# Performance work log

Measured on AMD Instinct MI355X. Metric: run time of the kernel, lower is better.

The kernel has to match this reference:

```python
import jax, jax.numpy as jnp
import numpy as np
from jax import lax

EPS = 1e-6


def layernorm2d(x, w, b):
    # channel LayerNorm over dim C of NCHW (biased variance), matching LayerNormFunction
    mu = jnp.mean(x, axis=1, keepdims=True)
    var = jnp.mean((x - mu) ** 2, axis=1, keepdims=True)
    y = (x - mu) * lax.rsqrt(var + EPS)
    return w[None, :, None, None] * y + b[None, :, None, None]


def conv1x1(x, W, b):
    # x: (N,C,H,W), W: (O,C), b: (O,)
    return jnp.einsum('nchw,oc->nohw', x, W) + b[None, :, None, None]


def conv3x3(x, W, b):
    # W: (O,I,3,3)
    y = lax.conv_general_dilated(x, W, window_strides=(1, 1), padding='SAME',
                                 dimension_numbers=('NCHW', 'OIHW', 'NCHW'))
    return y + b[None, :, None, None]


def avg_pool3x3(x):
    # torch F.avg_pool2d k=3, s=1, p=1, count_include_pad=True -> always divide by 9
    s = lax.reduce_window(x, 0.0, lax.add, (1, 1, 3, 3), (1, 1, 1, 1),
                          [(0, 0), (0, 0), (1, 1), (1, 1)])
    return s / 9.0


def setup_inputs() -> dict:
    key = jax.random.key(0)
    N, C, H, W = 8, 64, 128, 256
    ks = jax.random.split(key, 12)
    d = {
        'x_l': jax.random.normal(ks[0], (N, C, H, W), jnp.float32),
        'x_r': jax.random.normal(ks[1], (N, C, H, W), jnp.float32),
        'nl_w': jnp.ones((C,), jnp.float32),
        'nl_b': jnp.zeros((C,), jnp.float32),
        'nr_w': jnp.ones((C,), jnp.float32),
        'nr_b': jnp.zeros((C,), jnp.float32),
        'Wq_l': jax.random.normal(ks[2], (C, C), jnp.float32) * 0.05,
        'bq_l': jax.random.normal(ks[3], (C,), jnp.float32) * 0.05,
        'Wq_r': jax.random.normal(ks[4], (C, C), jnp.float32) * 0.05,
        'bq_r': jax.random.normal(ks[5], (C,), jnp.float32) * 0.05,
        'Wv_r': jax.random.normal(ks[6], (C, C), jnp.float32) * 0.05,
        'bv_r': jax.random.normal(ks[7], (C,), jnp.float32) * 0.05,
        'beta': jax.random.normal(ks[8], (1, C, 1, 1), jnp.float32) * 0.1,
        'gamma': jax.random.normal(ks[9], (1, C, 1, 1), jnp.float32) * 0.1,
        'W_hf': jax.random.normal(ks[10], (C, C, 3, 3), jnp.float32) * 0.02,
        'b_hf': jax.random.normal(ks[11], (C,), jnp.float32) * 0.02,
    }
    return d


def reference(x_l, x_r, nl_w, nl_b, nr_w, nr_b, Wq_l, bq_l, Wq_r, bq_r,
              Wv_r, bv_r, beta, gamma, W_hf, b_hf):
    C = x_l.shape[1]
    scale = C ** (-0.5)

    # Projections (1x1 convs); Q_l, Q_r, V_r as (N,H,W,C)
    Q_l = jnp.transpose(conv1x1(layernorm2d(x_l, nl_w, nl_b), Wq_l, bq_l), (0, 2, 3, 1))
    Q_r = jnp.transpose(conv1x1(layernorm2d(x_r, nr_w, nr_b), Wq_r, bq_r), (0, 2, 3, 1))
    V_r = jnp.transpose(conv1x1(x_r, Wv_r, bv_r), (0, 2, 3, 1))

    # Per-scanline cross attention: (N,H,W,W)
    attn = jnp.einsum('nhwc,nhvc->nhwv', Q_l, Q_r) * scale
    attn = jax.nn.softmax(attn, axis=-1)
    F_r2l = jnp.einsum('nhwv,nhvc->nhwc', attn, V_r)  # (N,H,W,C)
    F_r2l = jnp.transpose(F_r2l, (0, 3, 1, 2)) * beta  # (N,C,H,W)

    # High-frequency branch
    hf = conv3x3(x_r - avg_pool3x3(x_r), W_hf, b_hf)

    return x_l + F_r2l + gamma * hf
```

## Files before the change

### kernel.cpp

```cpp
#include <hip/hip_runtime.h>
#include <hip/hip_bf16.h>

#define N_ 8
#define C_ 64
#define H_ 128
#define W_ 256
#define HW_ (H_*W_)
#define CHW_ (C_*H_*W_)

typedef unsigned int u32;
typedef unsigned short u16;
typedef float f32x4 __attribute__((ext_vector_type(4)));
typedef short bf16x8 __attribute__((ext_vector_type(8)));

__device__ __forceinline__ float blo(u32 u) { return __uint_as_float(u << 16); }
__device__ __forceinline__ float bhi(u32 u) { return __uint_as_float(u & 0xffff0000u); }
__device__ __forceinline__ u16 f2bf(float f) {
    u32 u = __float_as_uint(f);
    u32 lsb = (u >> 16) & 1u;
    u += 0x7fffu + lsb;
    return (u16)(u >> 16);
}
__device__ __forceinline__ u32 pack2(float a, float b) {
    return (u32)f2bf(a) | ((u32)f2bf(b) << 16);
}
__device__ __forceinline__ int rmap(int px) {
    return (px & 0xF8) | ((px + (px >> 3)) & 7);
}

__global__ __launch_bounds__(512, 2) void k_fused(
    const float* __restrict__ xl, const float* __restrict__ xr,
    const float* __restrict__ nlw, const float* __restrict__ nlb,
    const float* __restrict__ nrw, const float* __restrict__ nrb,
    const float* __restrict__ Wql, const float* __restrict__ bql,
    const float* __restrict__ Wqr, const float* __restrict__ bqr,
    const float* __restrict__ Wvr, const float* __restrict__ bvr,
    const float* __restrict__ beta, float* __restrict__ out)
{
    __shared__ u32 B1[8192];
    __shared__ u32 B2[8192];
    __shared__ float muA[256], rsA[256];
    __shared__ float SlA[64], BlA[64], SrA[64], BrA[64], BvA[64];
    const int tid  = threadIdx.x;
    const int lane = tid & 63, wv = tid >> 6;
    const int l15  = lane & 15, kg = lane >> 4;
    const int mw   = wv & 3;
    const int nh   = wv >> 2;
    const int blk  = blockIdx.x;
    const int n = blk >> 7, h = blk & 127;
    const size_t gbase = (size_t)n*CHW_ + (size_t)h*W_;

    if (tid < 64) {
        const int o = tid;
        float sl = 0.f, bl = bql[o], sr = 0.f, br = bqr[o];
        for (int c = 0; c < 64; ++c) {
            float wl = Wql[o*64+c], wr = Wqr[o*64+c];
            sl += wl * nlw[c];
            bl += wl * nlb[c];
            sr += wr * nrw[c];
            br += wr * nrb[c];
        }
        SlA[o] = sl; BlA[o] = bl; SrA[o] = sr; BrA[o] = br; BvA[o] = bvr[o];
    }

    const int oA = mw*16 + l15;
    bf16x8 aL[2], aR[2], aV[2];
    #pragma unroll
    for (int hf = 0; hf < 2; ++hf) {
        bf16x8 tl, tr, tv;
        #pragma unroll
        for (int j = 0; j < 8; ++j) {
            const int c = hf*32 + kg*8 + j;
            tl[j] = (short)f2bf(Wql[oA*64+c] * nlw[c]);
            tr[j] = (short)f2bf(Wqr[oA*64+c] * nrw[c]);
            tv[j] = (short)f2bf(Wvr[oA*64+c]);
        }
        aL[hf] = tl; aR[hf] = tr; aV[hf] = tv;
    }

    const int schunk = tid >> 6;
    const int sj     = tid & 63;

    {
        const int c0 = schunk*8;
        float4 v[8];
        #pragma unroll
        for (int e = 0; e < 8; ++e)
            v[e] = *(const float4*)(xl + gbase + (size_t)(c0+e)*HW_ + sj*4);
        #pragma unroll
        for (int t = 0; t < 4; ++t) {
            const int px = sj*4 + t;
            const int r = rmap(px);
            u32 q0,q1,q2,q3;
            const float* f0 = (const float*)&v[0]; const float* f1 = (const float*)&v[1];
            const float* f2 = (const float*)&v[2]; const float* f3 = (const float*)&v[3];
            const float* f4 = (const float*)&v[4]; const float* f5 = (const float*)&v[5];
            const float* f6 = (const float*)&v[6]; const float* f7 = (const float*)&v[7];
            asm("v_cvt_pk_bf16_f32 %0, %1, %2" : "=v"(q0) : "v"(f0[t]), "v"(f1[t]));
            asm("v_cvt_pk_bf16_f32 %0, %1, %2" : "=v"(q1) : "v"(f2[t]), "v"(f3[t]));
            asm("v_cvt_pk_bf16_f32 %0, %1, %2" : "=v"(q2) : "v"(f4[t]), "v"(f5[t]));
            asm("v_cvt_pk_bf16_f32 %0, %1, %2" : "=v"(q3) : "v"(f6[t]), "v"(f7[t]));
            uint4 pv; pv.x=q0; pv.y=q1; pv.z=q2; pv.w=q3;
            *(uint4*)&B1[r*32 + ((schunk ^ (r&7))<<2)] = pv;
        }
    }
    float4 vr2[8];
    {
        const int c0 = schunk*8;
        #pragma unroll
        for (int e = 0; e < 8; ++e)
            vr2[e] = *(const float4*)(xr + gbase + (size_t)(c0+e)*HW_ + sj*4);
    }
    __syncthreads();
    if (tid < 256) {
        const int px = tid;
        const int r = rmap(px);
        float sum = 0.f, ssq = 0.f;
        #pragma unroll
        for (int c8 = 0; c8 < 8; ++c8) {
            uint4 val = *(const uint4*)&B1[r*32 + ((c8 ^ (r&7))<<2)];
            const u32* wp = (const u32*)&val;
            #pragma unroll
            for (int q = 0; q < 4; ++q) {
                float a = blo(wp[q]), b = bhi(wp[q]);
                sum += a + b; ssq += a*a + b*b;
            }
        }
        float mu = sum * (1.f/64.f);
        float var = ssq * (1.f/64.f) - mu*mu;
        muA[px] = mu;
        rsA[px] = rsqrtf(var + 1e-6f);
    }
    __syncthreads();
    {
        float Sv[4], Bv[4];
        #pragma unroll
        for (int r4 = 0; r4 < 4; ++r4) {
            Sv[r4] = SlA[mw*16 + kg*4 + r4];
            Bv[r4] = BlA[mw*16 + kg*4 + r4];
        }
        #pragma unroll
        for (int nt2 = 0; nt2 < 8; ++nt2) {
            const int nt = nh*8 + nt2;
            const int px = nt*16 + l15;
            const int r = rmap(px);
            f32x4 d = {0.f,0.f,0.f,0.f};
            #pragma unroll
            for (int hf = 0; hf < 2; ++hf) {
                bf16x8 b = *(const bf16x8*)&B1[r*32 + (((hf*4+kg) ^ (r&7))<<2)];
                d = __builtin_amdgcn_mfma_f32_16x16x32_bf16(aL[hf], b, d, 0, 0, 0);
            }
            const float mu = muA[px], rs = rsA[px];
            uint2 pv;
            pv.x = pack2(rs*(d[0] - mu*Sv[0]) + Bv[0], rs*(d[1] - mu*Sv[1]) + Bv[1]);
            pv.y = pack2(rs*(d[2] - mu*Sv[2]) + Bv[2], rs*(d[3] - mu*Sv[3]) + Bv[3]);
            const int ci = (mw*2 + (kg>>1)) ^ (px & 7);
            *(uint2*)&B2[px*32 + (ci<<2) + (kg&1)*2] = pv;
        }
    }
    __syncthreads();

    bf16x8 qf[2][2];
    #pragma unroll
    for (int ntq = 0; ntq < 2; ++ntq)
        #pragma unroll
        for (int ci = 0; ci < 2; ++ci) {
            const int q = wv*32 + ntq*16 + l15;
            qf[ntq][ci] = *(const bf16x8*)&B2[q*32 + (((ci*4+kg) ^ (q&7))<<2)];
        }
    {
        #pragma unroll
        for (int t = 0; t < 4; ++t) {
            const int px = sj*4 + t;
            const int r = rmap(px);
            u32 q0,q1,q2,q3;
            const float* f0 = (const float*)&vr2[0]; const float* f1 = (const float*)&vr2[1];
            const float* f2 = (const float*)&vr2[2]; const float* f3 = (const float*)&vr2[3];
            const float* f4 = (const float*)&vr2[4]; const float* f5 = (const float*)&vr2[5];
            const float* f6 = (const float*)&vr2[6]; const float* f7 = (const float*)&vr2[7];
            asm("v_cvt_pk_bf16_f32 %0, %1, %2" : "=v"(q0) : "v"(f0[t]), "v"(f1[t]));
            asm("v_cvt_pk_bf16_f32 %0, %1, %2" : "=v"(q1) : "v"(f2[t]), "v"(f3[t]));
            asm("v_cvt_pk_bf16_f32 %0, %1, %2" : "=v"(q2) : "v"(f4[t]), "v"(f5[t]));
            asm("v_cvt_pk_bf16_f32 %0, %1, %2" : "=v"(q3) : "v"(f6[t]), "v"(f7[t]));
            uint4 pv; pv.x=q0; pv.y=q1; pv.z=q2; pv.w=q3;
            *(uint4*)&B1[r*32 + ((schunk ^ (r&7))<<2)] = pv;
        }
    }
    __syncthreads();
    if (tid < 256) {
        const int px = tid;
        const int r = rmap(px);
        float sum = 0.f, ssq = 0.f;
        #pragma unroll
        for (int c8 = 0; c8 < 8; ++c8) {
            uint4 val = *(const uint4*)&B1[r*32 + ((c8 ^ (r&7))<<2)];
            const u32* wp = (const u32*)&val;
            #pragma unroll
            for (int q = 0; q < 4; ++q) {
                float a = blo(wp[q]), b = bhi(wp[q]);
                sum += a + b; ssq += a*a + b*b;
            }
        }
        float mu = sum * (1.f/64.f);
        float var = ssq * (1.f/64.f) - mu*mu;
        muA[px] = mu;
        rsA[px] = rsqrtf(var + 1e-6f);
    }
    __syncthreads();

    u32 hq[8][2], hv[8][2];
    {
        float Sv[4], Bv[4];
        #pragma unroll
        for (int r4 = 0; r4 < 4; ++r4) {
            Sv[r4] = SrA[mw*16 + kg*4 + r4];
            Bv[r4] = BrA[mw*16 + kg*4 + r4];
        }
        const int chv = mw*16 + l15;
        const float vbias = BvA[chv];
        #pragma unroll
        for (int nt2 = 0; nt2 < 8; ++nt2) {
            const int nt = nh*8 + nt2;
            const int px = nt*16 + l15;
            const int r = rmap(px);
            bf16x8 bX[2];
            #pragma unroll
            for (int hf = 0; hf < 2; ++hf)
                bX[hf] = *(const bf16x8*)&B1[r*32 + (((hf*4+kg) ^ (r&7))<<2)];
            f32x4 dq = {0.f,0.f,0.f,0.f};
            f32x4 dv = {0.f,0.f,0.f,0.f};
            #pragma unroll
            for (int hf = 0; hf < 2; ++hf) {
                dq = __builtin_amdgcn_mfma_f32_16x16x32_bf16(aR[hf], bX[hf], dq, 0, 0, 0);
                dv = __builtin_amdgcn_mfma_f32_16x16x32_bf16(bX[hf], aV[hf], dv, 0, 0, 0);
            }
            const float mu = muA[px], rs = rsA[px];
            hq[nt2][0] = pack2(rs*(dq[0] - mu*Sv[0]) + Bv[0], rs*(dq[1] - mu*Sv[1]) + Bv[1]);
            hq[nt2][1] = pack2(rs*(dq[2] - mu*Sv[2]) + Bv[2], rs*(dq[3] - mu*Sv[3]) + Bv[3]);
            hv[nt2][0] = pack2(dv[0] + vbias, dv[1] + vbias);
            hv[nt2][1] = pack2(dv[2] + vbias, dv[3] + vbias);
        }
    }
    __syncthreads();
    {
        const int chv = mw*16 + l15;
        u16* Vts16 = (u16*)B2;
        #pragma unroll
        for (int nt2 = 0; nt2 < 8; ++nt2) {
            const int nt = nh*8 + nt2;
            const int px = nt*16 + l15;
            const int ciq = (mw*2 + (kg>>1)) ^ (px & 7);
            uint2 pq; pq.x = hq[nt2][0]; pq.y = hq[nt2][1];
            *(uint2*)&B1[px*32 + (ciq<<2) + (kg&1)*2] = pq;
            uint2 pw; pw.x = hv[nt2][0]; pw.y = hv[nt2][1];
            const int swz = (nt*2 + (kg>>1)) ^ (chv & 7);
            *(uint2*)&Vts16[chv*256 + (swz<<3) + (kg&1)*4] = pw;
        }
    }
    __syncthreads();

    f32x4 oacc[2][4];
    #pragma unroll
    for (int a = 0; a < 2; ++a)
        #pragma unroll
        for (int b = 0; b < 4; ++b)
            oacc[a][b] = (f32x4){0.f,0.f,0.f,0.f};
    float lsum[2] = {0.f,0.f};
    const uint4* KsR = (const uint4*)B1;
    const u16* Vts = (const u16*)B2;
    const int srcA = ((2*kg) & 3)*16 + l15;

    for (int kb = 0; kb < 8; ++kb) {
        f32x4 st[2][2];
        #pragma unroll
        for (int mt = 0; mt < 2; ++mt)
            #pragma unroll
            for (int nt = 0; nt < 2; ++nt)
                st[mt][nt] = (f32x4){0.f,0.f,0.f,0.f};
        #pragma unroll
        for (int ci = 0; ci < 2; ++ci) {
            bf16x8 a0 = *(const bf16x8*)&KsR[(kb*32 +      l15)*8 + ((ci*4 + kg) ^ (l15 & 7))];
            bf16x8 a1 = *(const bf16x8*)&KsR[(kb*32 + 16 + l15)*8 + ((ci*4 + kg) ^ (l15 & 7))];
            #pragma unroll
            for (int nt = 0; nt < 2; ++nt) {
                st[0][nt] = __builtin_amdgcn_mfma_f32_16x16x32_bf16(a0, qf[nt][ci], st[0][nt], 0, 0, 0);
                st[1][nt] = __builtin_amdgcn_mfma_f32_16x16x32_bf16(a1, qf[nt][ci], st[1][nt], 0, 0, 0);
            }
        }
        bf16x8 paR[2];
        #pragma unroll
        for (int nt = 0; nt < 2; ++nt) {
            float p00 = __expf(st[0][nt][0]*0.125f);
            float p01 = __expf(st[0][nt][1]*0.125f);
            float p02 = __expf(st[0][nt][2]*0.125f);
            float p03 = __expf(st[0][nt][3]*0.125f);
            float p10 = __expf(st[1][nt][0]*0.125f);
            float p11 = __expf(st[1][nt][1]*0.125f);
            float p12 = __expf(st[1][nt][2]*0.125f);
            float p13 = __expf(st[1][nt][3]*0.125f);
            lsum[nt] += ((p00+p01)+(p02+p03)) + ((p10+p11)+(p12+p13));
            u32 pk00, pk01, pk10, pk11;
            asm("v_cvt_pk_bf16_f32 %0, %1, %2" : "=v"(pk00) : "v"(p00), "v"(p01));
            asm("v_cvt_pk_bf16_f32 %0, %1, %2" : "=v"(pk01) : "v"(p02), "v"(p03));
            asm("v_cvt_pk_bf16_f32 %0, %1, %2" : "=v"(pk10) : "v"(p10), "v"(p11));
            asm("v_cvt_pk_bf16_f32 %0, %1, %2" : "=v"(pk11) : "v"(p12), "v"(p13));
            int a00 = __shfl((int)pk00, srcA, 64);
            int a01 = __shfl((int)pk01, srcA, 64);
            int a10 = __shfl((int)pk10, srcA, 64);
            int a11 = __shfl((int)pk11, srcA, 64);
            int b00 = __shfl((int)pk00, srcA + 16, 64);
            int b01 = __shfl((int)pk01, srcA + 16, 64);
            int b10 = __shfl((int)pk10, srcA + 16, 64);
            int b11 = __shfl((int)pk11, srcA + 16, 64);
            const bool lo = (kg < 2);
            union { u32 u[4]; bf16x8 v; } pu;
            pu.u[0] = (u32)(lo ? a00 : a10);
            pu.u[1] = (u32)(lo ? a01 : a11);
            pu.u[2] = (u32)(lo ? b00 : b10);
            pu.u[3] = (u32)(lo ? b01 : b11);
            paR[nt] = pu.v;
        }
        bf16x8 vb[4];
        #pragma unroll
        for (int nc = 0; nc < 4; ++nc)
            vb[nc] = *(const bf16x8*)&Vts[(nc*16 + l15)*256 + ((kb*4 + kg) ^ (l15 & 7))*8];
        #pragma unroll
        for (int qt = 0; qt < 2; ++qt)
            #pragma unroll
            for (int nc = 0; nc < 4; ++nc)
                oacc[qt][nc] = __builtin_amdgcn_mfma_f32_16x16x32_bf16(paR[qt], vb[nc], oacc[qt][nc], 0, 0, 0);
    }

    #pragma unroll
    for (int nt = 0; nt < 2; ++nt) {
        float s = lsum[nt];
        s += __shfl_xor(s, 16, 64);
        s += __shfl_xor(s, 32, 64);
        lsum[nt] = s;
    }
    float linv[2][4];
    #pragma unroll
    for (int qt = 0; qt < 2; ++qt)
        #pragma unroll
        for (int r = 0; r < 4; ++r)
            linv[qt][r] = 1.0f / __shfl(lsum[qt], kg*4 + r, 64);

    const size_t qbase = gbase + wv*32;
    #pragma unroll
    for (int nc = 0; nc < 4; ++nc) {
        const int ch = nc*16 + l15;
        const float bch = beta[ch];
        #pragma unroll
        for (int qt = 0; qt < 2; ++qt) {
            const size_t gidx = qbase + (size_t)ch*HW_ + qt*16 + kg*4;
            f32x4 vals;
            #pragma unroll
            for (int r = 0; r < 4; ++r)
                vals[r] = bch*(oacc[qt][nc][r]*linv[qt][r]);
            *(f32x4*)&out[gidx] = vals;
        }
    }
}

__global__ __launch_bounds__(256) void k_hipass(
    const float* __restrict__ xr, u16* __restrict__ Tt)
{
    __shared__ u16 Ts[64*256];
    const int bid = blockIdx.x;
    const int blk = (bid & 7)*128 + (bid >> 3);
    const int n = blk >> 7, h = blk & 127;
    const int tid = threadIdx.x;
    const int lane = tid & 63, wv = tid >> 6;
    const float* rowp = xr + (size_t)n*CHW_ + (size_t)h*W_ + lane*4;

    #pragma unroll
    for (int ci = 0; ci < 16; ++ci) {
        const int c = wv*16 + ci;
        const float* pc = rowp + (size_t)c*HW_;
        float ctr0=0.f, ctr1=0.f, ctr2=0.f, ctr3=0.f;
        float s0=0.f, s1=0.f, s2=0.f, s3=0.f;
        #pragma unroll
        for (int dy = -1; dy <= 1; ++dy) {
            const int hh = h + dy;
            float4 v = {0.f,0.f,0.f,0.f};
            if (hh >= 0 && hh < 128) v = *(const float4*)(pc + dy*W_);
            float lft = __shfl_up(v.w, 1);
            float rgt = __shfl_down(v.x, 1);
            if (lane == 0)  lft = 0.f;
            if (lane == 63) rgt = 0.f;
            s0 += lft + v.x + v.y;
            s1 += v.x + v.y + v.z;
            s2 += v.y + v.z + v.w;
            s3 += v.z + v.w + rgt;
            if (dy == 0) { ctr0=v.x; ctr1=v.y; ctr2=v.z; ctr3=v.w; }
        }
        uint2 pv;
        pv.x = pack2(ctr0 - s0*(1.f/9.f), ctr1 - s1*(1.f/9.f));
        pv.y = pack2(ctr2 - s2*(1.f/9.f), ctr3 - s3*(1.f/9.f));
        const int swz = (c >> 3) << 3;
        *(uint2*)&Ts[c*256 + ((lane*4) ^ swz)] = pv;
    }
    __syncthreads();
    uint4* gout = (uint4*)(Tt + (size_t)blk*256*64);
    #pragma unroll
    for (int iter = 0; iter < 8; ++iter) {
        const int lin = iter*256 + tid;
        const int px = lin >> 3, chunk = lin & 7;
        const int pxs = px ^ (chunk << 3);
        u32 w4[4];
        #pragma unroll
        for (int tp = 0; tp < 4; ++tp) {
            const int c0 = chunk*8 + tp*2;
            u16 a = Ts[(c0    )*256 + pxs];
            u16 b = Ts[(c0 + 1)*256 + pxs];
            w4[tp] = (u32)a | ((u32)b << 16);
        }
        uint4 v; v.x=w4[0]; v.y=w4[1]; v.z=w4[2]; v.w=w4[3];
        gout[lin] = v;
    }
}

__device__ __forceinline__ void conv_tile(
    const uint4* __restrict__ buf, const bf16x8* A,
    const float* gv, const float* bv,
    int n, int h, int w0, int mt, int l15, int kg,
    const float* __restrict__ xl, float* __restrict__ out)
{
    f32x4 acc[4] = {{0,0,0,0},{0,0,0,0},{0,0,0,0},{0,0,0,0}};
    #pragma unroll
    for (int s = 0; s < 18; ++s) {
        const int q  = s >> 1;
        const int dy = q / 3, dx = q % 3;
        const int c0 = (s & 1)*4 + kg;
        #pragma unroll
        for (int nt = 0; nt < 4; ++nt) {
            const int wt = nt*16 + l15 + dx;
            bf16x8 b = *(const bf16x8*)&buf[(dy*66 + wt)*8 + (c0 ^ (wt & 7))];
            acc[nt] = __builtin_amdgcn_mfma_f32_16x16x32_bf16(A[s], b, acc[nt], 0, 0, 0);
        }
    }
    #pragma unroll
    for (int nt = 0; nt < 4; ++nt) {
        const int px = w0 + nt*16 + l15;
        #pragma unroll
        for (int r = 0; r < 4; ++r) {
            const int oo = mt*16 + kg*4 + r;
            size_t idx = (size_t)(n*64 + oo)*HW_ + (size_t)h*W_ + px;
            out[idx] = out[idx] + xl[idx] + gv[r]*(acc[nt][r] + bv[r]);
        }
    }
}

__global__ __launch_bounds__(256) void k_conv(
    const u16* __restrict__ Tt, const float* __restrict__ Whf,
    const float* __restrict__ bhf, const float* __restrict__ gam,
    const float* __restrict__ xl, float* __restrict__ out)
{
    __shared__ uint4 Xs[2][1584];
    const int tid  = threadIdx.x;
    const int lane = tid & 63;
    const int mt   = tid >> 6;
    const int l15  = lane & 15;
    const int kg   = lane >> 4;
    const int bid  = blockIdx.x;
    const int blk2 = (bid & 7)*256 + (bid >> 3);
    const int row  = blk2 >> 1, half = blk2 & 1;
    const int n = row >> 7, h = row & 127;
    const int w00 = half*128;
    const int w01 = w00 + 64;

    const int oa = mt*16 + l15;
    bf16x8 A[18];
    #pragma unroll
    for (int s = 0; s < 18; ++s) {
        const int q  = s >> 1;
        const int ib = (s & 1)*32 + kg*8;
        bf16x8 a;
        #pragma unroll
        for (int j = 0; j < 8; ++j) {
            float wv = Whf[(size_t)(oa*64 + ib + j)*9 + q];
            a[j] = (short)f2bf(wv);
        }
        A[s] = a;
    }
    float gv[4], bv[4];
    #pragma unroll
    for (int r = 0; r < 4; ++r) {
        int oo = mt*16 + kg*4 + r;
        gv[r] = gam[oo];
        bv[r] = bhf[oo];
    }

    for (int it = tid; it < 1584; it += 256) {
        int dy    = it / 528;
        int rem   = it - dy*528;
        int wt    = rem >> 3;
        int chunk = rem & 7;
        int hh = h + dy - 1;
        int wg = w00 + wt - 1;
        uint4 v = {0,0,0,0};
        if (hh >= 0 && hh < 128 && wg >= 0 && wg < 256)
            v = *(const uint4*)(Tt + (((size_t)(n*128 + hh)*256 + wg)*64 + chunk*8));
        Xs[0][(dy*66 + wt)*8 + (chunk ^ (wt & 7))] = v;
    }
    __syncthreads();

    uint4 rr[7];
    #pragma unroll
    for (int k = 0; k < 7; ++k) {
        const int it = k*256 + tid;
        if (it < 1584) {
            int dy    = it / 528;
            int rem   = it - dy*528;
            int wt    = rem >> 3;
            int chunk = rem & 7;
            int hh = h + dy - 1;
            int wg = w01 + wt - 1;
            uint4 v = {0,0,0,0};
            if (hh >= 0 && hh < 128 && wg >= 0 && wg < 256)
                v = *(const uint4*)(Tt + (((size_t)(n*128 + hh)*256 + wg)*64 + chunk*8));
            rr[k] = v;
        }
    }

    conv_tile(&Xs[0][0], A, gv, bv, n, h, w00, mt, l15, kg, xl, out);

    #pragma unroll
    for (int k = 0; k < 7; ++k) {
        const int it = k*256 + tid;
        if (it < 1584) {
            int dy    = it / 528;
            int rem   = it - dy*528;
            int wt    = rem >> 3;
            int chunk = rem & 7;
            Xs[1][(dy*66 + wt)*8 + (chunk ^ (wt & 7))] = rr[k];
        }
    }
    __syncthreads();
    conv_tile(&Xs[1][0], A, gv, bv, n, h, w01, mt, l15, kg, xl, out);
}

extern "C" void kernel_launch(void* const* d_in, const int* in_sizes, int n_in,
                              void* d_out, int out_size, void* d_ws, size_t ws_size,
                              hipStream_t stream)
{
    const float* xl   = (const float*)d_in[0];
    const float* xr   = (const float*)d_in[1];
    const float* nlw  = (const float*)d_in[2];
    const float* nlb  = (const float*)d_in[3];
    const float* nrw  = (const float*)d_in[4];
    const float* nrb  = (const float*)d_in[5];
    const float* Wql  = (const float*)d_in[6];
    const float* bql  = (const float*)d_in[7];
    const float* Wqr  = (const float*)d_in[8];
    const float* bqr  = (const float*)d_in[9];
    const float* Wvr  = (const float*)d_in[10];
    const float* bvr  = (const float*)d_in[11];
    const float* beta = (const float*)d_in[12];
    const float* gam  = (const float*)d_in[13];
    const float* Whf  = (const float*)d_in[14];
    const float* bhf  = (const float*)d_in[15];
    float* out = (float*)d_out;

    u16* Tt = (u16*)d_ws;

    k_hipass<<<1024, 256, 0, stream>>>(xr, Tt);
    k_fused<<<1024, 512, 0, stream>>>(xl, xr, nlw, nlb, nrw, nrb,
                                      Wql, bql, Wqr, bqr, Wvr, bvr,
                                      beta, out);
    k_conv<<<2048, 256, 0, stream>>>(Tt, Whf, bhf, gam, xl, out);
}
```

Measured before the change: 193.8 us.

## Merge high-pass kernel into attention kernel via block roles; move x_l residual add

The separate high-pass kernel is folded into the attention kernel as a second block role: odd blocks compute the x_r minus avg-pool bf16 tile, even blocks run attention, so the two workloads share one launch and can overlap on the GPU. The x_l residual add moves from the conv kernel's read-modify-write into the attention epilogue, so the conv kernel no longer reads x_l. This removes one launch and lets the memory-bound high-pass blocks run alongside the compute-heavy attention blocks. In exchange, the high-pass blocks now launch with 512 threads and the large shared-memory footprint of the attention kernel, which may reduce occupancy for that role.

```diff
diff --git a/kernel.cpp b/kernel.cpp
--- a/kernel.cpp
+++ b/kernel.cpp
@@ -28,25 +28,84 @@
     return (px & 0xF8) | ((px + (px >> 3)) & 7);
 }
 
-__global__ __launch_bounds__(512, 2) void k_fused(
+__global__ __launch_bounds__(512, 2) void k_main(
     const float* __restrict__ xl, const float* __restrict__ xr,
     const float* __restrict__ nlw, const float* __restrict__ nlb,
     const float* __restrict__ nrw, const float* __restrict__ nrb,
     const float* __restrict__ Wql, const float* __restrict__ bql,
     const float* __restrict__ Wqr, const float* __restrict__ bqr,
     const float* __restrict__ Wvr, const float* __restrict__ bvr,
-    const float* __restrict__ beta, float* __restrict__ out)
+    const float* __restrict__ beta, u16* __restrict__ Tt,
+    float* __restrict__ out)
 {
     __shared__ u32 B1[8192];
     __shared__ u32 B2[8192];
     __shared__ float muA[256], rsA[256];
     __shared__ float SlA[64], BlA[64], SrA[64], BrA[64], BvA[64];
-    const int tid  = threadIdx.x;
+    const int tid = threadIdx.x;
+    const int bid = blockIdx.x;
+    const int role = bid & 1;
+    const int sub  = bid >> 1;
+
+    if (role == 1) {
+        u16* Ts = (u16*)B1;
+        const int blkh = (sub & 7)*128 + (sub >> 3);
+        const int nh_ = blkh >> 7, hh_ = blkh & 127;
+        const int lane = tid & 63, wvv = tid >> 6;
+        const float* rowp = xr + (size_t)nh_*CHW_ + (size_t)hh_*W_ + lane*4;
+        #pragma unroll
+        for (int ci = 0; ci < 8; ++ci) {
+            const int c = wvv*8 + ci;
+            const float* pc = rowp + (size_t)c*HW_;
+            float ctr0=0.f, ctr1=0.f, ctr2=0.f, ctr3=0.f;
+            float s0=0.f, s1=0.f, s2=0.f, s3=0.f;
+            #pragma unroll
+            for (int dy = -1; dy <= 1; ++dy) {
+                const int hh2 = hh_ + dy;
+                float4 v = {0.f,0.f,0.f,0.f};
+                if (hh2 >= 0 && hh2 < 128) v = *(const float4*)(pc + dy*W_);
+                float lft = __shfl_up(v.w, 1);
+                float rgt = __shfl_down(v.x, 1);
+                if (lane == 0)  lft = 0.f;
+                if (lane == 63) rgt = 0.f;
+                s0 += lft + v.x + v.y;
+                s1 += v.x + v.y + v.z;
+                s2 += v.y + v.z + v.w;
+                s3 += v.z + v.w + rgt;
+                if (dy == 0) { ctr0=v.x; ctr1=v.y; ctr2=v.z; ctr3=v.w; }
+            }
+            uint2 pv;
+            pv.x = pack2(ctr0 - s0*(1.f/9.f), ctr1 - s1*(1.f/9.f));
+            pv.y = pack2(ctr2 - s2*(1.f/9.f), ctr3 - s3*(1.f/9.f));
+            const int swz = (c >> 3) << 3;
+            *(uint2*)&Ts[c*256 + ((lane*4) ^ swz)] = pv;
+        }
+        __syncthreads();
+        uint4* gout = (uint4*)(Tt + (size_t)blkh*256*64);
+        #pragma unroll
+        for (int iter = 0; iter < 4; ++iter) {
+            const int lin = iter*512 + tid;
+            const int px = lin >> 3, chunk = lin & 7;
+            const int pxs = px ^ (chunk << 3);
+            u32 w4[4];
+            #pragma unroll
+            for (int tp = 0; tp < 4; ++tp) {
+                const int c0 = chunk*8 + tp*2;
+                u16 a = Ts[(c0    )*256 + pxs];
+                u16 b = Ts[(c0 + 1)*256 + pxs];
+                w4[tp] = (u32)a | ((u32)b << 16);
+            }
+            uint4 v; v.x=w4[0]; v.y=w4[1]; v.z=w4[2]; v.w=w4[3];
+            gout[lin] = v;
+        }
+        return;
+    }
+
     const int lane = tid & 63, wv = tid >> 6;
     const int l15  = lane & 15, kg = lane >> 4;
     const int mw   = wv & 3;
     const int nh   = wv >> 2;
-    const int blk  = blockIdx.x;
+    const int blk  = sub;
     const int n = blk >> 7, h = blk & 127;
     const size_t gbase = (size_t)n*CHW_ + (size_t)h*W_;
 
@@ -353,70 +412,13 @@
         #pragma unroll
         for (int qt = 0; qt < 2; ++qt) {
             const size_t gidx = qbase + (size_t)ch*HW_ + qt*16 + kg*4;
+            f32x4 x4 = *(const f32x4*)&xl[gidx];
             f32x4 vals;
             #pragma unroll
             for (int r = 0; r < 4; ++r)
-                vals[r] = bch*(oacc[qt][nc][r]*linv[qt][r]);
+                vals[r] = x4[r] + bch*(oacc[qt][nc][r]*linv[qt][r]);
             *(f32x4*)&out[gidx] = vals;
         }
-    }
-}
-
-__global__ __launch_bounds__(256) void k_hipass(
-    const float* __restrict__ xr, u16* __restrict__ Tt)
-{
-    __shared__ u16 Ts[64*256];
-    const int bid = blockIdx.x;
-    const int blk = (bid & 7)*128 + (bid >> 3);
-    const int n = blk >> 7, h = blk & 127;
-    const int tid = threadIdx.x;
-    const int lane = tid & 63, wv = tid >> 6;
-    const float* rowp = xr + (size_t)n*CHW_ + (size_t)h*W_ + lane*4;
-
-    #pragma unroll
-    for (int ci = 0; ci < 16; ++ci) {
-        const int c = wv*16 + ci;
-        const float* pc = rowp + (size_t)c*HW_;
-        float ctr0=0.f, ctr1=0.f, ctr2=0.f, ctr3=0.f;
-        float s0=0.f, s1=0.f, s2=0.f, s3=0.f;
-        #pragma unroll
-        for (int dy = -1; dy <= 1; ++dy) {
-            const int hh = h + dy;
-            float4 v = {0.f,0.f,0.f,0.f};
-            if (hh >= 0 && hh < 128) v = *(const float4*)(pc + dy*W_);
-            float lft = __shfl_up(v.w, 1);
-            float rgt = __shfl_down(v.x, 1);
-            if (lane == 0)  lft = 0.f;
-            if (lane == 63) rgt = 0.f;
-            s0 += lft + v.x + v.y;
-            s1 += v.x + v.y + v.z;
-            s2 += v.y + v.z + v.w;
-            s3 += v.z + v.w + rgt;
-            if (dy == 0) { ctr0=v.x; ctr1=v.y; ctr2=v.z; ctr3=v.w; }
-        }
-        uint2 pv;
-        pv.x = pack2(ctr0 - s0*(1.f/9.f), ctr1 - s1*(1.f/9.f));
-        pv.y = pack2(ctr2 - s2*(1.f/9.f), ctr3 - s3*(1.f/9.f));
-        const int swz = (c >> 3) << 3;
-        *(uint2*)&Ts[c*256 + ((lane*4) ^ swz)] = pv;
-    }
-    __syncthreads();
-    uint4* gout = (uint4*)(Tt + (size_t)blk*256*64);
-    #pragma unroll
-    for (int iter = 0; iter < 8; ++iter) {
-        const int lin = iter*256 + tid;
-        const int px = lin >> 3, chunk = lin & 7;
-        const int pxs = px ^ (chunk << 3);
-        u32 w4[4];
-        #pragma unroll
-        for (int tp = 0; tp < 4; ++tp) {
-            const int c0 = chunk*8 + tp*2;
-            u16 a = Ts[(c0    )*256 + pxs];
-            u16 b = Ts[(c0 + 1)*256 + pxs];
-            w4[tp] = (u32)a | ((u32)b << 16);
-        }
-        uint4 v; v.x=w4[0]; v.y=w4[1]; v.z=w4[2]; v.w=w4[3];
-        gout[lin] = v;
     }
 }
 
@@ -424,7 +426,7 @@
     const uint4* __restrict__ buf, const bf16x8* A,
     const float* gv, const float* bv,
     int n, int h, int w0, int mt, int l15, int kg,
-    const float* __restrict__ xl, float* __restrict__ out)
+    float* __restrict__ out)
 {
     f32x4 acc[4] = {{0,0,0,0},{0,0,0,0},{0,0,0,0},{0,0,0,0}};
     #pragma unroll
@@ -446,7 +448,7 @@
         for (int r = 0; r < 4; ++r) {
             const int oo = mt*16 + kg*4 + r;
             size_t idx = (size_t)(n*64 + oo)*HW_ + (size_t)h*W_ + px;
-            out[idx] = out[idx] + xl[idx] + gv[r]*(acc[nt][r] + bv[r]);
+            out[idx] += gv[r]*(acc[nt][r] + bv[r]);
         }
     }
 }
@@ -454,7 +456,7 @@
 __global__ __launch_bounds__(256) void k_conv(
     const u16* __restrict__ Tt, const float* __restrict__ Whf,
     const float* __restrict__ bhf, const float* __restrict__ gam,
-    const float* __restrict__ xl, float* __restrict__ out)
+    float* __restrict__ out)
 {
     __shared__ uint4 Xs[2][1584];
     const int tid  = threadIdx.x;
@@ -523,7 +525,7 @@
         }
     }
 
-    conv_tile(&Xs[0][0], A, gv, bv, n, h, w00, mt, l15, kg, xl, out);
+    conv_tile(&Xs[0][0], A, gv, bv, n, h, w00, mt, l15, kg, out);
 
     #pragma unroll
     for (int k = 0; k < 7; ++k) {
@@ -537,7 +539,7 @@
         }
     }
     __syncthreads();
-    conv_tile(&Xs[1][0], A, gv, bv, n, h, w01, mt, l15, kg, xl, out);
+    conv_tile(&Xs[1][0], A, gv, bv, n, h, w01, mt, l15, kg, out);
 }
 
 extern "C" void kernel_launch(void* const* d_in, const int* in_sizes, int n_in,
@@ -564,9 +566,8 @@
 
     u16* Tt = (u16*)d_ws;
 
-    k_hipass<<<1024, 256, 0, stream>>>(xr, Tt);
-    k_fused<<<1024, 512, 0, stream>>>(xl, xr, nlw, nlb, nrw, nrb,
-                                      Wql, bql, Wqr, bqr, Wvr, bvr,
-                                      beta, out);
-    k_conv<<<2048, 256, 0, stream>>>(Tt, Whf, bhf, gam, xl, out);
-}
+    k_main<<<2048, 512, 0, stream>>>(xl, xr, nlw, nlb, nrw, nrb,
+                                     Wql, bql, Wqr, bqr, Wvr, bvr,
+                                     beta, Tt, out);
+    k_conv<<<2048, 256, 0, stream>>>(Tt, Whf, bhf, gam, out);
+}
```

After: 222.9 us. 1.15x slower.
